# Performance work log

Measured on AMD Instinct MI355X. Metric: run time of the kernel, lower is better.

Reference implementation:

```python
import jax, jax.numpy as jnp
import numpy as np

B, L, D, H, M = 2, 1024, 1024, 16, 64
DH = D // H  # depth per head


def setup_inputs() -> dict:
    key = jax.random.key(0)
    ks = jax.random.split(key, 7)
    s = 0.02
    return {
        "x": jax.random.normal(ks[0], (B, L, D), jnp.float32),
        "Wq": jax.random.normal(ks[1], (D, D), jnp.float32) * s,
        "Wk": jax.random.normal(ks[2], (D, D), jnp.float32) * s,
        "Wv": jax.random.normal(ks[3], (D, D), jnp.float32) * s,
        "Wo": jax.random.normal(ks[4], (D, D), jnp.float32) * s,
        "rel_k_table": jax.random.normal(ks[5], (2 * M + 1, DH), jnp.float32) * s,
        "rel_v_table": jax.random.normal(ks[6], (2 * M + 1, DH), jnp.float32) * s,
    }


def _rel_idx(length, max_rel):
    # Shaw-style clipped relative position indices: [L, L] in [0, 2*max_rel]
    r = jnp.arange(length)
    return jnp.clip(r[None, :] - r[:, None], -max_rel, max_rel) + max_rel


def _split_heads(t):
    # [B, L, D] -> [B, H, L, DH]
    return t.reshape(B, L, H, DH).transpose(0, 2, 1, 3)


def reference(x, Wq, Wk, Wv, Wo, rel_k_table, rel_v_table):
    q = _split_heads(x @ Wq) * (DH ** -0.5)  # T2T scales q by d_head^-0.5
    k = _split_heads(x @ Wk)
    v = _split_heads(x @ Wv)

    idx = _rel_idx(L, M)
    rel_k = rel_k_table[idx]  # [L, L, DH] gathered keys-relative embeddings
    rel_v = rel_v_table[idx]  # [L, L, DH]

    # _relative_attention_inner(q, k, rel_k, transpose=True)
    logits = jnp.einsum('bhid,bhjd->bhij', q, k) + jnp.einsum('bhid,ijd->bhij', q, rel_k)
    w = jax.nn.softmax(logits, axis=-1)  # [B, H, L, L]; dropout_rate=0 / inference

    # _relative_attention_inner(w, v, rel_v, transpose=False)
    o = jnp.einsum('bhij,bhjd->bhid', w, v) + jnp.einsum('bhij,ijd->bhid', w, rel_v)

    # combine heads then output transform
    o = o.transpose(0, 2, 1, 3).reshape(B, L, D)
    return o @ Wo
```

## Files before the change

### kernel.cpp

```cpp
#include <hip/hip_runtime.h>
#include <hip/hip_bf16.h>
#include <math.h>

#define B_ 2
#define L_ 1024
#define D_ 1024
#define H_ 16
#define DH_ 64
#define M_ 64
#define R_ 129
#define NLD ((size_t)B_ * L_ * D_)
#define DD  ((size_t)D_ * D_)
#define QSCALE 0.18033688011112042f

using bf16x8 = __attribute__((ext_vector_type(8))) short;
using f32x4  = __attribute__((ext_vector_type(4))) float;

__device__ __forceinline__ unsigned short f2bf(float f) {
    unsigned int x = __builtin_bit_cast(unsigned int, f);
    unsigned int r = x + 0x7fffu + ((x >> 16) & 1u);
    return (unsigned short)(r >> 16);
}
__device__ __forceinline__ float bf2f(unsigned short u) {
    unsigned int x = ((unsigned int)u) << 16;
    return __builtin_bit_cast(float, x);
}
__device__ __forceinline__ unsigned int pk2bf(float lo, float hi) {
    __hip_bfloat162 h = __float22bfloat162_rn(float2{lo, hi});
    unsigned int u;
    __builtin_memcpy(&u, &h, 4);
    return u;
}

__global__ __launch_bounds__(256)
void prep(const float* __restrict__ x,
          const float* __restrict__ W0, const float* __restrict__ W1,
          const float* __restrict__ W2, const float* __restrict__ W3,
          const float* __restrict__ relk, const float* __restrict__ relv,
          unsigned short* __restrict__ xb, unsigned short* __restrict__ Wt,
          unsigned short* __restrict__ relkb, unsigned short* __restrict__ relvT)
{
    __shared__ float tile[32][33];
    const int bid = blockIdx.x, t = threadIdx.x;
    if (bid < 2048) {
        const int i = bid * 256 + t;
        float4 v = ((const float4*)x)[i];
        short4 o = { (short)f2bf(v.x), (short)f2bf(v.y), (short)f2bf(v.z), (short)f2bf(v.w) };
        ((short4*)xb)[i] = o;
    } else if (bid < 6144) {
        const int wb = bid - 2048;
        const int z = wb >> 10, rem = wb & 1023;
        const float* W = z == 0 ? W0 : z == 1 ? W1 : z == 2 ? W2 : W3;
        unsigned short* T = Wt + (size_t)z * DD;
        const int k0 = (rem >> 5) * 32, n0 = (rem & 31) * 32;
        const int r = t >> 3, c = (t & 7) * 4;
        float4 v = *(const float4*)&W[(size_t)(k0 + r) * D_ + n0 + c];
        tile[r][c] = v.x; tile[r][c + 1] = v.y; tile[r][c + 2] = v.z; tile[r][c + 3] = v.w;
        __syncthreads();
        short4 o = { (short)f2bf(tile[c][r]),     (short)f2bf(tile[c + 1][r]),
                     (short)f2bf(tile[c + 2][r]), (short)f2bf(tile[c + 3][r]) };
        *(short4*)&T[(size_t)(n0 + r) * D_ + k0 + c] = o;
    } else {
        const int idx = (bid - 6144) * 256 + t;
        if (idx < 144 * 64) {
            const int r = idx >> 6, d = idx & 63;
            relkb[idx] = (r < R_) ? f2bf(relk[r * 64 + d]) : (unsigned short)0;
        }
        if (idx < 64 * 136) {
            const int d = idx / 136, r = idx - d * 136;
            relvT[idx] = (r < R_) ? f2bf(relv[r * 64 + d]) : (unsigned short)0;
        }
    }
}

__global__ __launch_bounds__(256)
void gemm64(const unsigned short* __restrict__ A, const unsigned short* __restrict__ Bt,
            unsigned short* __restrict__ Cb, float* __restrict__ Cf, float scale0)
{
    __shared__ unsigned short As[64][64];
    __shared__ unsigned short Bs[128][64];

    const int t = threadIdx.x, lane = t & 63, wid = t >> 6;
    const int fr = lane & 15, g = lane >> 4;
    const int m0 = blockIdx.y * 64;
    const int nglob = blockIdx.x * 128;
    const int mat = nglob >> 10;
    const int n0 = nglob & 1023;
    const float scale = (mat == 0) ? scale0 : 1.f;
    const int wm = (wid >> 1) * 32, wn = (wid & 1) * 64;

    f32x4 acc[2][4] = {};

    int arow[2], akof[2], adst[2];
#pragma unroll
    for (int c = 0; c < 2; ++c) {
        const int chunk = c * 256 + t;
        arow[c] = chunk >> 3;
        akof[c] = ((chunk & 7) ^ (arow[c] & 7)) * 8;
        adst[c] = chunk * 8;
    }
    int brow[4], bkof[4], bdst[4];
#pragma unroll
    for (int c = 0; c < 4; ++c) {
        const int chunk = c * 256 + t;
        brow[c] = chunk >> 3;
        bkof[c] = ((chunk & 7) ^ (brow[c] & 7)) * 8;
        bdst[c] = chunk * 8;
    }

    const unsigned short* Abase = A  + (size_t)m0 * D_;
    const unsigned short* Bbase = Bt + (size_t)nglob * D_;

    for (int k0 = 0; k0 < D_; k0 += 64) {
        __syncthreads();
#pragma unroll
        for (int c = 0; c < 2; ++c)
            __builtin_amdgcn_global_load_lds(
                (const __attribute__((address_space(1))) void*)(Abase + (size_t)arow[c] * D_ + k0 + akof[c]),
                (__attribute__((address_space(3))) void*)(&As[0][0] + adst[c]), 16, 0, 0);
#pragma unroll
        for (int c = 0; c < 4; ++c)
            __builtin_amdgcn_global_load_lds(
                (const __attribute__((address_space(1))) void*)(Bbase + (size_t)brow[c] * D_ + k0 + bkof[c]),
                (__attribute__((address_space(3))) void*)(&Bs[0][0] + bdst[c]), 16, 0, 0);
        __syncthreads();

#pragma unroll
        for (int kb = 0; kb < 2; ++kb) {
            bf16x8 av[2], bv[4];
#pragma unroll
            for (int i = 0; i < 2; ++i) {
                const int ra = wm + i * 16 + fr;
                av[i] = *(const bf16x8*)&As[ra][(((kb << 2) + g) ^ (ra & 7)) * 8];
            }
#pragma unroll
            for (int j = 0; j < 4; ++j) {
                const int rb = wn + j * 16 + fr;
                bv[j] = *(const bf16x8*)&Bs[rb][(((kb << 2) + g) ^ (rb & 7)) * 8];
            }
#pragma unroll
            for (int i = 0; i < 2; ++i)
#pragma unroll
                for (int j = 0; j < 4; ++j)
                    acc[i][j] = __builtin_amdgcn_mfma_f32_16x16x32_bf16(av[i], bv[j], acc[i][j], 0, 0, 0);
        }
    }

    const int orow = g * 4;
    if (Cb) {
        unsigned short* Cp = Cb + (size_t)mat * NLD;
#pragma unroll
        for (int i = 0; i < 2; ++i)
#pragma unroll
            for (int j = 0; j < 4; ++j) {
                unsigned short* cp = Cp + (size_t)(m0 + wm + i * 16 + orow) * D_ + n0 + wn + j * 16 + fr;
#pragma unroll
                for (int rg = 0; rg < 4; ++rg)
                    cp[(size_t)rg * D_] = f2bf(acc[i][j][rg] * scale);
            }
    } else {
#pragma unroll
        for (int i = 0; i < 2; ++i)
#pragma unroll
            for (int j = 0; j < 4; ++j) {
                float* cp = Cf + (size_t)(m0 + wm + i * 16 + orow) * D_ + n0 + wn + j * 16 + fr;
#pragma unroll
                for (int rg = 0; rg < 4; ++rg)
                    cp[(size_t)rg * D_] = acc[i][j][rg] * scale;
            }
    }
}

__device__ __forceinline__ void stage_k(const unsigned short* src, unsigned short* dst, int t)
{
#pragma unroll
    for (int it = 0; it < 2; ++it) {
        const int c = it * 256 + t;
        const int j = c >> 3;
        const int sc = (c & 7) ^ (j & 7);
        __builtin_amdgcn_global_load_lds(
            (const __attribute__((address_space(1))) void*)(src + (size_t)j * D_ + sc * 8),
            (__attribute__((address_space(3))) void*)(dst + c * 8), 16, 0, 0);
    }
}

__device__ __forceinline__ void write_vt(unsigned short (*Vtl)[64], int jp, int d0, bf16x8 a, bf16x8 b)
{
    const int jlo = (2 * jp) & 7;
    const int jc  = jp >> 2;
#pragma unroll
    for (int e = 0; e < 8; ++e) {
        const int d = d0 + e;
        const unsigned int val = (unsigned int)(unsigned short)a[e]
                               | ((unsigned int)(unsigned short)b[e] << 16);
        *(unsigned int*)&Vtl[d][((jc ^ (d & 7)) << 3) + jlo] = val;
    }
}

__global__ __launch_bounds__(256)
void attn_mfma(const unsigned short* __restrict__ Qb, const unsigned short* __restrict__ Kb,
               const unsigned short* __restrict__ Vb,
               const unsigned short* __restrict__ relkb,
               const unsigned short* __restrict__ relvT,
               const float* __restrict__ relv,
               unsigned short* __restrict__ Ob)
{
    __shared__ unsigned short Klds[3][64][64];
    __shared__ unsigned short Vt[2][64][64];
    __shared__ unsigned short Plds[64][72];
    __shared__ unsigned short QW[64][136];

    const int t    = threadIdx.x;
    const int lane = t & 63;
    const int w    = t >> 6;
    const int fr   = lane & 15;
    const int g    = lane >> 4;

    const int bx  = blockIdx.x;
    const int xcd = bx & 7, slot = bx >> 3;
    const int bh  = (xcd << 2) | (slot >> 4);
    const int rb  = slot & 15;
    const int b   = bh >> 4, h = bh & 15;
    const int i0  = rb * 64;
    const size_t head = (size_t)b * L_ * D_ + (size_t)h * DH_;

    const int iloc = w * 16 + fr;

    const unsigned short* Kh = Kb + head;
    const unsigned short* Vh = Vb + head;

    stage_k(Kh, &Klds[0][0][0], t);
    stage_k(Kh + (size_t)64 * D_, &Klds[1][0][0], t);

    const int jp = t & 31, d0v = ((t >> 5) & 7) * 8;
    bf16x8 va, vb2;
    {
        const unsigned short* vsrc = Vh + (size_t)(2 * jp) * D_ + d0v;
        asm volatile("global_load_dwordx4 %0, %1, off" : "=v"(va)  : "v"(vsrc)      : "memory");
        asm volatile("global_load_dwordx4 %0, %1, off" : "=v"(vb2) : "v"(vsrc + D_) : "memory");
    }

    bf16x8 qf[2];
    {
        const unsigned short* qp = Qb + head + (size_t)(i0 + iloc) * D_;
        qf[0] = *(const bf16x8*)(qp + g * 8);
        qf[1] = *(const bf16x8*)(qp + 32 + g * 8);
    }

#pragma unroll
    for (int rc = 0; rc < 9; ++rc) {
        f32x4 acc = {};
#pragma unroll
        for (int kb = 0; kb < 2; ++kb) {
            bf16x8 rv = *(const bf16x8*)&relkb[(size_t)(rc * 16 + fr) * 64 + kb * 32 + g * 8];
            acc = __builtin_amdgcn_mfma_f32_16x16x32_bf16(rv, qf[kb], acc, 0, 0, 0);
        }
        if (rc < 8) {
            uint2 pk = { pk2bf(acc[0], acc[1]), pk2bf(acc[2], acc[3]) };
            *(uint2*)&QW[iloc][rc * 16 + g * 4] = pk;
        } else if (g == 0) {
            QW[iloc][128] = f2bf(acc[0]);
        }
    }
    if (rb == 0) {
        for (int c = 1 + g; c <= 63 - iloc; c += 4) QW[iloc][c] = 0;
    } else if (rb == 15) {
        for (int c = 128 - iloc + g; c <= 127; c += 4) QW[iloc][c] = 0;
    }

    asm volatile("s_waitcnt vmcnt(0)" ::: "memory");
    __builtin_amdgcn_sched_barrier(0);
    write_vt(Vt[0], jp, d0v, va, vb2);
    __syncthreads();

    const float qr0   = bf2f(QW[iloc][0]);
    const float qr128 = bf2f(QW[iloc][128]);

    f32x4 oacc[4] = {};
    float lpart = 0.f, pe0p = 0.f, pe128p = 0.f;

    int kcur = 0;
    for (int jt = 0; jt < 16; ++jt) {
        if (jt < 15) {
            const unsigned short* vsrc = Vh + (size_t)((jt + 1) * 64 + 2 * jp) * D_ + d0v;
            asm volatile("global_load_dwordx4 %0, %1, off" : "=v"(va)  : "v"(vsrc)      : "memory");
            asm volatile("global_load_dwordx4 %0, %1, off" : "=v"(vb2) : "v"(vsrc + D_) : "memory");
        }
        if (jt < 14) {
            int kpre = kcur + 2; if (kpre >= 3) kpre -= 3;
            stage_k(Kh + (size_t)(jt + 2) * 64 * D_, &Klds[kpre][0][0], t);
        }

        f32x4 s[4];
        __builtin_amdgcn_s_setprio(1);
#pragma unroll
        for (int fc = 0; fc < 4; ++fc) {
            f32x4 a = {};
            const int j = fc * 16 + fr;
#pragma unroll
            for (int kb = 0; kb < 2; ++kb) {
                bf16x8 kv = *(const bf16x8*)&Klds[kcur][j][(((kb << 2) + g) ^ (j & 7)) * 8];
                a = __builtin_amdgcn_mfma_f32_16x16x32_bf16(kv, qf[kb], a, 0, 0, 0);
            }
            s[fc] = a;
        }
        __builtin_amdgcn_s_setprio(0);

        bf16x8 vv0[4], vv1[4];
#pragma unroll
        for (int fd = 0; fd < 4; ++fd) {
            const int d = fd * 16 + fr;
            vv0[fd] = *(const bf16x8*)&Vt[jt & 1][d][((g)     ^ (d & 7)) * 8];
            vv1[fd] = *(const bf16x8*)&Vt[jt & 1][d][((4 + g) ^ (d & 7)) * 8];
        }

        const int dt   = (jt - rb) * 64;
        const int relb = dt - iloc + g * 4;

        if (dt <= -128 || dt >= 128) {
            const float qrc = (dt < 0) ? qr0 : qr128;
            float tsum = 0.f;
#pragma unroll
            for (int fc = 0; fc < 4; ++fc) {
                float p0 = exp2f(s[fc][0] + qrc);
                float p1 = exp2f(s[fc][1] + qrc);
                float p2 = exp2f(s[fc][2] + qrc);
                float p3 = exp2f(s[fc][3] + qrc);
                uint2 pk = { pk2bf(p0, p1), pk2bf(p2, p3) };
                *(uint2*)&Plds[iloc][fc * 16 + g * 4] = pk;
                tsum += (p0 + p1) + (p2 + p3);
            }
            lpart += tsum;
            if (dt < 0) pe0p += tsum; else pe128p += tsum;
        } else if (dt == 0) {
#pragma unroll
            for (int fc = 0; fc < 4; ++fc) {
                const int c0 = relb + fc * 16 + M_;
                float pe[4];
#pragma unroll
                for (int reg = 0; reg < 4; ++reg) {
                    pe[reg] = exp2f(s[fc][reg] + bf2f(QW[iloc][c0 + reg]));
                    lpart += pe[reg];
                }
                uint2 pk = { pk2bf(pe[0], pe[1]), pk2bf(pe[2], pe[3]) };
                *(uint2*)&Plds[iloc][fc * 16 + g * 4] = pk;
                QW[iloc][c0 + 0] = (unsigned short)(pk.x & 0xffffu);
                QW[iloc][c0 + 1] = (unsigned short)(pk.x >> 16);
                QW[iloc][c0 + 2] = (unsigned short)(pk.y & 0xffffu);
                QW[iloc][c0 + 3] = (unsigned short)(pk.y >> 16);
            }
        } else {
#pragma unroll
            for (int fc = 0; fc < 4; ++fc) {
                float pe[4];
#pragma unroll
                for (int reg = 0; reg < 4; ++reg) {
                    const int colr = relb + fc * 16 + reg + M_;
                    const int col  = colr < 0 ? 0 : (colr > 128 ? 128 : colr);
                    const float bias = (col == 0) ? qr0 : (col == 128) ? qr128
                                                        : bf2f(QW[iloc][col]);
                    pe[reg] = exp2f(s[fc][reg] + bias);
                    lpart += pe[reg];
                    if (col == 0)        pe0p   += pe[reg];
                    else if (col == 128) pe128p += pe[reg];
                    else                 QW[iloc][col] = f2bf(pe[reg]);
                }
                uint2 pk = { pk2bf(pe[0], pe[1]), pk2bf(pe[2], pe[3]) };
                *(uint2*)&Plds[iloc][fc * 16 + g * 4] = pk;
            }
        }

        asm volatile("s_waitcnt lgkmcnt(0)" ::: "memory");
        __builtin_amdgcn_sched_barrier(0);

        bf16x8 pa0 = *(const bf16x8*)&Plds[iloc][g * 8];
        bf16x8 pa1 = *(const bf16x8*)&Plds[iloc][32 + g * 8];
        __builtin_amdgcn_s_setprio(1);
#pragma unroll
        for (int fd = 0; fd < 4; ++fd) {
            oacc[fd] = __builtin_amdgcn_mfma_f32_16x16x32_bf16(pa0, vv0[fd], oacc[fd], 0, 0, 0);
            oacc[fd] = __builtin_amdgcn_mfma_f32_16x16x32_bf16(pa1, vv1[fd], oacc[fd], 0, 0, 0);
        }
        __builtin_amdgcn_s_setprio(0);

        if (jt < 15) {
            if (jt < 14) asm volatile("s_waitcnt vmcnt(2)" ::: "memory");
            else         asm volatile("s_waitcnt vmcnt(0)" ::: "memory");
            __builtin_amdgcn_sched_barrier(0);
            write_vt(Vt[(jt + 1) & 1], jp, d0v, va, vb2);
        }
        asm volatile("s_waitcnt lgkmcnt(0)" ::: "memory");
        __builtin_amdgcn_s_barrier();
        kcur = (kcur == 2) ? 0 : kcur + 1;
    }

    lpart  += __shfl_xor(lpart, 16);  lpart  += __shfl_xor(lpart, 32);
    pe0p   += __shfl_xor(pe0p, 16);   pe0p   += __shfl_xor(pe0p, 32);
    pe128p += __shfl_xor(pe128p, 16); pe128p += __shfl_xor(pe128p, 32);
    if (g == 0) {
        QW[iloc][0]   = f2bf(pe0p);
        QW[iloc][128] = f2bf(pe128p);
    }
    asm volatile("s_waitcnt lgkmcnt(0)" ::: "memory");
    __builtin_amdgcn_sched_barrier(0);

#pragma unroll
    for (int kc = 0; kc < 4; ++kc) {
        bf16x8 wa = *(const bf16x8*)&QW[iloc][kc * 32 + g * 8];
#pragma unroll
        for (int fd = 0; fd < 4; ++fd) {
            bf16x8 rv = *(const bf16x8*)&relvT[(size_t)(fd * 16 + fr) * 136 + kc * 32 + g * 8];
            oacc[fd] = __builtin_amdgcn_mfma_f32_16x16x32_bf16(wa, rv, oacc[fd], 0, 0, 0);
        }
    }

    float invd[4], pr128[4];
#pragma unroll
    for (int reg = 0; reg < 4; ++reg) {
        const int src = (lane & 48) | (g * 4 + reg);
        invd[reg]  = 1.f / __shfl(lpart, src, 64);
        pr128[reg] = __shfl(pe128p, src, 64);
    }

#pragma unroll
    for (int fd = 0; fd < 4; ++fd) {
        const float r128 = relv[128 * 64 + fd * 16 + fr];
        unsigned short* op = Ob + head + (size_t)(i0 + w * 16 + g * 4) * D_ + fd * 16 + fr;
#pragma unroll
        for (int reg = 0; reg < 4; ++reg)
            op[(size_t)reg * D_] = f2bf((oacc[fd][reg] + pr128[reg] * r128) * invd[reg]);
    }
}

extern "C" void kernel_launch(void* const* d_in, const int* in_sizes, int n_in,
                              void* d_out, int out_size, void* d_ws, size_t ws_size,
                              hipStream_t stream)
{
    const float* x    = (const float*)d_in[0];
    const float* Wq   = (const float*)d_in[1];
    const float* Wk   = (const float*)d_in[2];
    const float* Wv   = (const float*)d_in[3];
    const float* Wo   = (const float*)d_in[4];
    const float* relk = (const float*)d_in[5];
    const float* relv = (const float*)d_in[6];
    float* out = (float*)d_out;

    unsigned short* xb    = (unsigned short*)d_ws;
    unsigned short* Wt    = xb + NLD;
    unsigned short* relkb = Wt + 4 * DD;
    unsigned short* relvT = relkb + 144 * 64;
    unsigned short* QKVb  = relvT + 64 * 136;
    unsigned short* Ob    = QKVb + 3 * NLD;

    prep<<<dim3(6180), 256, 0, stream>>>(x, Wq, Wk, Wv, Wo, relk, relv, xb, Wt, relkb, relvT);

    gemm64<<<dim3(24, 32), 256, 0, stream>>>(xb, Wt, QKVb, nullptr, QSCALE);

    attn_mfma<<<dim3(512), 256, 0, stream>>>(QKVb, QKVb + NLD, QKVb + 2 * NLD,
                                             relkb, relvT, relv, Ob);

    gemm64<<<dim3(8, 32), 256, 0, stream>>>(Ob, Wt + 3 * DD, nullptr, out, 1.f);
}
```

Baseline: 84.07 us.

## Split attention work across waves by key rows instead of query rows

The attention kernel is restructured so each wave owns a 16-key slice of every 64-key tile across all 64 queries, rather than owning 16 queries. The P tile stays in registers and is fed straight into 16x16x16 MFMAs, which removes the Plds round-trip through shared memory. The cost is moved to the end: partial output accumulators and softmax sums have to be reduced across waves through LDS with extra barriers. The Q·relK bias computation is also spread over the waves, and launch bounds now request 2 blocks per CU. Register pressure rises, since oacc grows to 16 f32x4 and qf to 8 bf16x8.

New measurement: 89.75 us (median of 4 runs). 1.07x slower.

```diff
diff --git a/kernel.cpp b/kernel.cpp
--- a/kernel.cpp
+++ b/kernel.cpp
@@ -14,6 +14,7 @@
 #define QSCALE 0.18033688011112042f
 
 using bf16x8 = __attribute__((ext_vector_type(8))) short;
+using bf16x4 = __attribute__((ext_vector_type(4))) short;
 using f32x4  = __attribute__((ext_vector_type(4))) float;
 
 __device__ __forceinline__ unsigned short f2bf(float f) {
@@ -30,6 +31,15 @@
     unsigned int u;
     __builtin_memcpy(&u, &h, 4);
     return u;
+}
+__device__ __forceinline__ bf16x4 mkbf4(float a, float b, float c, float d) {
+    unsigned long long v = (unsigned long long)pk2bf(a, b)
+                         | ((unsigned long long)pk2bf(c, d) << 32);
+    return __builtin_bit_cast(bf16x4, v);
+}
+__device__ __forceinline__ f32x4 mfma16(bf16x4 a, bf16x4 b, f32x4 c) {
+    asm("v_mfma_f32_16x16x16_bf16 %0, %1, %2, %0" : "+v"(c) : "v"(a), "v"(b));
+    return c;
 }
 
 __global__ __launch_bounds__(256)
@@ -197,7 +207,7 @@
     }
 }
 
-__global__ __launch_bounds__(256)
+__global__ __launch_bounds__(256, 2)
 void attn_mfma(const unsigned short* __restrict__ Qb, const unsigned short* __restrict__ Kb,
                const unsigned short* __restrict__ Vb,
                const unsigned short* __restrict__ relkb,
@@ -205,10 +215,10 @@
                const float* __restrict__ relv,
                unsigned short* __restrict__ Ob)
 {
-    __shared__ unsigned short Klds[3][64][64];
-    __shared__ unsigned short Vt[2][64][64];
-    __shared__ unsigned short Plds[64][72];
+    __shared__ __align__(16) unsigned short Klds[3][64][64];
+    __shared__ __align__(16) unsigned short Vt[2][64][64];
     __shared__ unsigned short QW[64][136];
+    __shared__ float lredL[4][4][16], lredP0[4][4][16], lredP128[4][4][16];
 
     const int t    = threadIdx.x;
     const int lane = t & 63;
@@ -224,8 +234,6 @@
     const int i0  = rb * 64;
     const size_t head = (size_t)b * L_ * D_ + (size_t)h * DH_;
 
-    const int iloc = w * 16 + fr;
-
     const unsigned short* Kh = Kb + head;
     const unsigned short* Vh = Vb + head;
 
@@ -240,32 +248,52 @@
         asm volatile("global_load_dwordx4 %0, %1, off" : "=v"(vb2) : "v"(vsrc + D_) : "memory");
     }
 
-    bf16x8 qf[2];
+    bf16x8 qf[4][2];
+#pragma unroll
+    for (int c = 0; c < 4; ++c) {
+        const unsigned short* qp = Qb + head + (size_t)(i0 + c * 16 + fr) * D_;
+        qf[c][0] = *(const bf16x8*)(qp + g * 8);
+        qf[c][1] = *(const bf16x8*)(qp + 32 + g * 8);
+    }
+
+    auto qr_rc = [&](int rc) {
+#pragma unroll
+        for (int c = 0; c < 4; ++c) {
+            f32x4 acc = {};
+#pragma unroll
+            for (int kb = 0; kb < 2; ++kb) {
+                bf16x8 rv = *(const bf16x8*)&relkb[(size_t)(rc * 16 + fr) * 64 + kb * 32 + g * 8];
+                acc = __builtin_amdgcn_mfma_f32_16x16x32_bf16(rv, qf[c][kb], acc, 0, 0, 0);
+            }
+            if (rc < 8) {
+                unsigned long long pk = (unsigned long long)pk2bf(acc[0], acc[1])
+                                      | ((unsigned long long)pk2bf(acc[2], acc[3]) << 32);
+                *(unsigned long long*)&QW[c * 16 + fr][rc * 16 + g * 4] = pk;
+            } else if (g == 0) {
+                QW[c * 16 + fr][128] = f2bf(acc[0]);
+            }
+        }
+    };
+    if      (w == 0) { qr_rc(0); qr_rc(4); qr_rc(8); }
+    else if (w == 1) { qr_rc(1); qr_rc(5); }
+    else if (w == 2) { qr_rc(2); qr_rc(6); }
+    else             { qr_rc(3); qr_rc(7); }
+
+    __syncthreads();
+
     {
-        const unsigned short* qp = Qb + head + (size_t)(i0 + iloc) * D_;
-        qf[0] = *(const bf16x8*)(qp + g * 8);
-        qf[1] = *(const bf16x8*)(qp + 32 + g * 8);
-    }
-
-#pragma unroll
-    for (int rc = 0; rc < 9; ++rc) {
-        f32x4 acc = {};
-#pragma unroll
-        for (int kb = 0; kb < 2; ++kb) {
-            bf16x8 rv = *(const bf16x8*)&relkb[(size_t)(rc * 16 + fr) * 64 + kb * 32 + g * 8];
-            acc = __builtin_amdgcn_mfma_f32_16x16x32_bf16(rv, qf[kb], acc, 0, 0, 0);
-        }
-        if (rc < 8) {
-            uint2 pk = { pk2bf(acc[0], acc[1]), pk2bf(acc[2], acc[3]) };
-            *(uint2*)&QW[iloc][rc * 16 + g * 4] = pk;
-        } else if (g == 0) {
-            QW[iloc][128] = f2bf(acc[0]);
-        }
-    }
-    if (rb == 0) {
-        for (int c = 1 + g; c <= 63 - iloc; c += 4) QW[iloc][c] = 0;
-    } else if (rb == 15) {
-        for (int c = 128 - iloc + g; c <= 127; c += 4) QW[iloc][c] = 0;
+        const int zrow = w * 16 + fr;
+        if (rb == 0) {
+            for (int c = 1 + g; c <= 63 - zrow; c += 4) QW[zrow][c] = 0;
+        } else if (rb == 15) {
+            for (int c = 128 - zrow + g; c <= 127; c += 4) QW[zrow][c] = 0;
+        }
+    }
+    float qr0[4], qr128[4];
+#pragma unroll
+    for (int c = 0; c < 4; ++c) {
+        qr0[c]   = bf2f(QW[c * 16 + fr][0]);
+        qr128[c] = bf2f(QW[c * 16 + fr][128]);
     }
 
     asm volatile("s_waitcnt vmcnt(0)" ::: "memory");
@@ -273,11 +301,8 @@
     write_vt(Vt[0], jp, d0v, va, vb2);
     __syncthreads();
 
-    const float qr0   = bf2f(QW[iloc][0]);
-    const float qr128 = bf2f(QW[iloc][128]);
-
-    f32x4 oacc[4] = {};
-    float lpart = 0.f, pe0p = 0.f, pe128p = 0.f;
+    f32x4 oacc[4][4] = {};
+    float lpart[4] = {}, pe0p[4] = {}, pe128p[4] = {};
 
     int kcur = 0;
     for (int jt = 0; jt < 16; ++jt) {
@@ -291,96 +316,78 @@
             stage_k(Kh + (size_t)(jt + 2) * 64 * D_, &Klds[kpre][0][0], t);
         }
 
+        const int jrow = w * 16 + fr;
+        bf16x8 kv0 = *(const bf16x8*)&Klds[kcur][jrow][((g)     ^ (fr & 7)) * 8];
+        bf16x8 kv1 = *(const bf16x8*)&Klds[kcur][jrow][((4 + g) ^ (fr & 7)) * 8];
+        bf16x4 vt4[4];
+#pragma unroll
+        for (int fd = 0; fd < 4; ++fd) {
+            const int d = fd * 16 + fr;
+            vt4[fd] = *(const bf16x4*)&Vt[jt & 1][d][((((w << 1) + (g >> 1)) ^ (d & 7)) << 3) + (g & 1) * 4];
+        }
+
         f32x4 s[4];
         __builtin_amdgcn_s_setprio(1);
 #pragma unroll
-        for (int fc = 0; fc < 4; ++fc) {
+        for (int c = 0; c < 4; ++c) {
             f32x4 a = {};
-            const int j = fc * 16 + fr;
-#pragma unroll
-            for (int kb = 0; kb < 2; ++kb) {
-                bf16x8 kv = *(const bf16x8*)&Klds[kcur][j][(((kb << 2) + g) ^ (j & 7)) * 8];
-                a = __builtin_amdgcn_mfma_f32_16x16x32_bf16(kv, qf[kb], a, 0, 0, 0);
-            }
-            s[fc] = a;
+            a = __builtin_amdgcn_mfma_f32_16x16x32_bf16(kv0, qf[c][0], a, 0, 0, 0);
+            a = __builtin_amdgcn_mfma_f32_16x16x32_bf16(kv1, qf[c][1], a, 0, 0, 0);
+            s[c] = a;
         }
         __builtin_amdgcn_s_setprio(0);
 
-        bf16x8 vv0[4], vv1[4];
-#pragma unroll
-        for (int fd = 0; fd < 4; ++fd) {
-            const int d = fd * 16 + fr;
-            vv0[fd] = *(const bf16x8*)&Vt[jt & 1][d][((g)     ^ (d & 7)) * 8];
-            vv1[fd] = *(const bf16x8*)&Vt[jt & 1][d][((4 + g) ^ (d & 7)) * 8];
-        }
-
-        const int dt   = (jt - rb) * 64;
-        const int relb = dt - iloc + g * 4;
-
-        if (dt <= -128 || dt >= 128) {
-            const float qrc = (dt < 0) ? qr0 : qr128;
-            float tsum = 0.f;
-#pragma unroll
-            for (int fc = 0; fc < 4; ++fc) {
-                float p0 = exp2f(s[fc][0] + qrc);
-                float p1 = exp2f(s[fc][1] + qrc);
-                float p2 = exp2f(s[fc][2] + qrc);
-                float p3 = exp2f(s[fc][3] + qrc);
-                uint2 pk = { pk2bf(p0, p1), pk2bf(p2, p3) };
-                *(uint2*)&Plds[iloc][fc * 16 + g * 4] = pk;
-                tsum += (p0 + p1) + (p2 + p3);
-            }
-            lpart += tsum;
-            if (dt < 0) pe0p += tsum; else pe128p += tsum;
-        } else if (dt == 0) {
-#pragma unroll
-            for (int fc = 0; fc < 4; ++fc) {
-                const int c0 = relb + fc * 16 + M_;
+        const int base_u = (jt - rb) * 64 + w * 16;
+        bf16x4 pb[4];
+#pragma unroll
+        for (int c = 0; c < 4; ++c) {
+            const int u   = base_u - c * 16;
+            const int row = c * 16 + fr;
+            float p0, p1, p2, p3;
+            if (u <= -80 || u >= 80) {
+                const float qrc = (u < 0) ? qr0[c] : qr128[c];
+                p0 = exp2f(s[c][0] + qrc); p1 = exp2f(s[c][1] + qrc);
+                p2 = exp2f(s[c][2] + qrc); p3 = exp2f(s[c][3] + qrc);
+                const float ts = (p0 + p1) + (p2 + p3);
+                lpart[c] += ts;
+                if (u < 0) pe0p[c] += ts; else pe128p[c] += ts;
+            } else if (u >= -48 && u <= 48) {
+                const int cb = u + 64 - fr + g * 4;
+                p0 = exp2f(s[c][0] + bf2f(QW[row][cb]));
+                p1 = exp2f(s[c][1] + bf2f(QW[row][cb + 1]));
+                p2 = exp2f(s[c][2] + bf2f(QW[row][cb + 2]));
+                p3 = exp2f(s[c][3] + bf2f(QW[row][cb + 3]));
+                lpart[c] += (p0 + p1) + (p2 + p3);
+                QW[row][cb]     = f2bf(p0);
+                QW[row][cb + 1] = f2bf(p1);
+                QW[row][cb + 2] = f2bf(p2);
+                QW[row][cb + 3] = f2bf(p3);
+            } else {
                 float pe[4];
 #pragma unroll
-                for (int reg = 0; reg < 4; ++reg) {
-                    pe[reg] = exp2f(s[fc][reg] + bf2f(QW[iloc][c0 + reg]));
-                    lpart += pe[reg];
+                for (int e = 0; e < 4; ++e) {
+                    const int colr = u + 64 - fr + g * 4 + e;
+                    const int col  = colr < 0 ? 0 : (colr > 128 ? 128 : colr);
+                    const float bias = (col == 0) ? qr0[c]
+                                     : (col == 128) ? qr128[c]
+                                     : bf2f(QW[row][col]);
+                    pe[e] = exp2f(s[c][e] + bias);
+                    lpart[c] += pe[e];
+                    if (col == 0)        pe0p[c]   += pe[e];
+                    else if (col == 128) pe128p[c] += pe[e];
+                    else                 QW[row][col] = f2bf(pe[e]);
                 }
-                uint2 pk = { pk2bf(pe[0], pe[1]), pk2bf(pe[2], pe[3]) };
-                *(uint2*)&Plds[iloc][fc * 16 + g * 4] = pk;
-                QW[iloc][c0 + 0] = (unsigned short)(pk.x & 0xffffu);
-                QW[iloc][c0 + 1] = (unsigned short)(pk.x >> 16);
-                QW[iloc][c0 + 2] = (unsigned short)(pk.y & 0xffffu);
-                QW[iloc][c0 + 3] = (unsigned short)(pk.y >> 16);
-            }
-        } else {
-#pragma unroll
-            for (int fc = 0; fc < 4; ++fc) {
-                float pe[4];
-#pragma unroll
-                for (int reg = 0; reg < 4; ++reg) {
-                    const int colr = relb + fc * 16 + reg + M_;
-                    const int col  = colr < 0 ? 0 : (colr > 128 ? 128 : colr);
-                    const float bias = (col == 0) ? qr0 : (col == 128) ? qr128
-                                                        : bf2f(QW[iloc][col]);
-                    pe[reg] = exp2f(s[fc][reg] + bias);
-                    lpart += pe[reg];
-                    if (col == 0)        pe0p   += pe[reg];
-                    else if (col == 128) pe128p += pe[reg];
-                    else                 QW[iloc][col] = f2bf(pe[reg]);
-                }
-                uint2 pk = { pk2bf(pe[0], pe[1]), pk2bf(pe[2], pe[3]) };
-                *(uint2*)&Plds[iloc][fc * 16 + g * 4] = pk;
-            }
-        }
-
-        asm volatile("s_waitcnt lgkmcnt(0)" ::: "memory");
-        __builtin_amdgcn_sched_barrier(0);
-
-        bf16x8 pa0 = *(const bf16x8*)&Plds[iloc][g * 8];
-        bf16x8 pa1 = *(const bf16x8*)&Plds[iloc][32 + g * 8];
+                p0 = pe[0]; p1 = pe[1]; p2 = pe[2]; p3 = pe[3];
+            }
+            pb[c] = mkbf4(p0, p1, p2, p3);
+        }
+
         __builtin_amdgcn_s_setprio(1);
 #pragma unroll
-        for (int fd = 0; fd < 4; ++fd) {
-            oacc[fd] = __builtin_amdgcn_mfma_f32_16x16x32_bf16(pa0, vv0[fd], oacc[fd], 0, 0, 0);
-            oacc[fd] = __builtin_amdgcn_mfma_f32_16x16x32_bf16(pa1, vv1[fd], oacc[fd], 0, 0, 0);
-        }
+        for (int fd = 0; fd < 4; ++fd)
+#pragma unroll
+            for (int c = 0; c < 4; ++c)
+                oacc[fd][c] = mfma16(vt4[fd], pb[c], oacc[fd][c]);
         __builtin_amdgcn_s_setprio(0);
 
         if (jt < 15) {
@@ -394,41 +401,80 @@
         kcur = (kcur == 2) ? 0 : kcur + 1;
     }
 
-    lpart  += __shfl_xor(lpart, 16);  lpart  += __shfl_xor(lpart, 32);
-    pe0p   += __shfl_xor(pe0p, 16);   pe0p   += __shfl_xor(pe0p, 32);
-    pe128p += __shfl_xor(pe128p, 16); pe128p += __shfl_xor(pe128p, 32);
-    if (g == 0) {
-        QW[iloc][0]   = f2bf(pe0p);
-        QW[iloc][128] = f2bf(pe128p);
-    }
-    asm volatile("s_waitcnt lgkmcnt(0)" ::: "memory");
-    __builtin_amdgcn_sched_barrier(0);
+#pragma unroll
+    for (int c = 0; c < 4; ++c) {
+        lpart[c]  += __shfl_xor(lpart[c], 16);  lpart[c]  += __shfl_xor(lpart[c], 32);
+        pe0p[c]   += __shfl_xor(pe0p[c], 16);   pe0p[c]   += __shfl_xor(pe0p[c], 32);
+        pe128p[c] += __shfl_xor(pe128p[c], 16); pe128p[c] += __shfl_xor(pe128p[c], 32);
+    }
+    if (lane < 16) {
+#pragma unroll
+        for (int c = 0; c < 4; ++c) {
+            lredL[w][c][fr]   = lpart[c];
+            lredP0[w][c][fr]  = pe0p[c];
+            lredP128[w][c][fr]= pe128p[c];
+        }
+    }
+    __syncthreads();
+    float lt[4], p0t[4], p128t[4];
+#pragma unroll
+    for (int c = 0; c < 4; ++c) {
+        lt[c]    = (lredL[0][c][fr] + lredL[1][c][fr]) + (lredL[2][c][fr] + lredL[3][c][fr]);
+        p0t[c]   = (lredP0[0][c][fr] + lredP0[1][c][fr]) + (lredP0[2][c][fr] + lredP0[3][c][fr]);
+        p128t[c] = (lredP128[0][c][fr] + lredP128[1][c][fr]) + (lredP128[2][c][fr] + lredP128[3][c][fr]);
+    }
+    if (w == 0 && g == 0) {
+#pragma unroll
+        for (int c = 0; c < 4; ++c) {
+            QW[c * 16 + fr][0]   = f2bf(p0t[c]);
+            QW[c * 16 + fr][128] = f2bf(p128t[c]);
+        }
+    }
+    __syncthreads();
 
 #pragma unroll
     for (int kc = 0; kc < 4; ++kc) {
-        bf16x8 wa = *(const bf16x8*)&QW[iloc][kc * 32 + g * 8];
-#pragma unroll
-        for (int fd = 0; fd < 4; ++fd) {
-            bf16x8 rv = *(const bf16x8*)&relvT[(size_t)(fd * 16 + fr) * 136 + kc * 32 + g * 8];
-            oacc[fd] = __builtin_amdgcn_mfma_f32_16x16x32_bf16(wa, rv, oacc[fd], 0, 0, 0);
-        }
-    }
-
-    float invd[4], pr128[4];
-#pragma unroll
-    for (int reg = 0; reg < 4; ++reg) {
-        const int src = (lane & 48) | (g * 4 + reg);
-        invd[reg]  = 1.f / __shfl(lpart, src, 64);
-        pr128[reg] = __shfl(pe128p, src, 64);
-    }
-
-#pragma unroll
+        bf16x8 rv = *(const bf16x8*)&relvT[(size_t)(w * 16 + fr) * 136 + kc * 32 + g * 8];
+#pragma unroll
+        for (int c = 0; c < 4; ++c) {
+            bf16x8 wa = *(const bf16x8*)&QW[c * 16 + fr][kc * 32 + g * 8];
+            oacc[w][c] = __builtin_amdgcn_mfma_f32_16x16x32_bf16(rv, wa, oacc[w][c], 0, 0, 0);
+        }
+    }
+
+    float* scr = (float*)&Klds[0][0][0];
     for (int fd = 0; fd < 4; ++fd) {
-        const float r128 = relv[128 * 64 + fd * 16 + fr];
-        unsigned short* op = Ob + head + (size_t)(i0 + w * 16 + g * 4) * D_ + fd * 16 + fr;
-#pragma unroll
-        for (int reg = 0; reg < 4; ++reg)
-            op[(size_t)reg * D_] = f2bf((oacc[fd][reg] + pr128[reg] * r128) * invd[reg]);
+        if (w != fd) {
+            const int sI = w - (w > fd ? 1 : 0);
+#pragma unroll
+            for (int c = 0; c < 4; ++c)
+                *(f32x4*)&scr[(sI * 4 + c) * 256 + lane * 4] = oacc[fd][c];
+        }
+        __syncthreads();
+        if (w == fd) {
+#pragma unroll
+            for (int c = 0; c < 4; ++c)
+#pragma unroll
+                for (int sI = 0; sI < 3; ++sI)
+                    oacc[fd][c] += *(const f32x4*)&scr[(sI * 4 + c) * 256 + lane * 4];
+        }
+        __syncthreads();
+    }
+
+    float r128[4];
+#pragma unroll
+    for (int reg = 0; reg < 4; ++reg)
+        r128[reg] = relv[128 * 64 + w * 16 + g * 4 + reg];
+#pragma unroll
+    for (int c = 0; c < 4; ++c) {
+        const float inv = 1.f / lt[c];
+        float v0 = (oacc[w][c][0] + p128t[c] * r128[0]) * inv;
+        float v1 = (oacc[w][c][1] + p128t[c] * r128[1]) * inv;
+        float v2 = (oacc[w][c][2] + p128t[c] * r128[2]) * inv;
+        float v3 = (oacc[w][c][3] + p128t[c] * r128[3]) * inv;
+        unsigned long long pk = (unsigned long long)pk2bf(v0, v1)
+                              | ((unsigned long long)pk2bf(v2, v3) << 32);
+        *(unsigned long long*)&Ob[head + (size_t)(i0 + c * 16 + fr) * D_ + w * 16 + g * 4] = pk;
     }
 }
 
```
